# Performance work log

Measured on AMD Instinct MI355X. Metric: run time of the kernel, lower is better.

Reference implementation:

```python
import jax, jax.numpy as jnp
import numpy as np

SEQ, B, IN, H, L = 512, 64, 128, 256, 6
STDV = 1.0 / (H ** 0.5)


def setup_inputs() -> dict:
    key = jax.random.key(0)
    ks = jax.random.split(key, 7)
    return {
        "x": jax.random.normal(ks[0], (SEQ, B, IN), jnp.float32),
        "h0": jax.random.normal(ks[1], (L, B, H), jnp.float32),
        "w_ih0": jax.random.uniform(ks[2], (3 * H, IN), jnp.float32, -STDV, STDV),
        "w_ih_rest": jax.random.uniform(ks[3], (L - 1, 3 * H, H), jnp.float32, -STDV, STDV),
        "w_hh": jax.random.uniform(ks[4], (L, 3 * H, H), jnp.float32, -STDV, STDV),
        "b_ih": jax.random.uniform(ks[5], (L, 3 * H), jnp.float32, -STDV, STDV),
        "b_hh": jax.random.uniform(ks[6], (L, 3 * H), jnp.float32, -STDV, STDV),
    }


def _gru_layer(x, h0, w_ih, w_hh, b_ih, b_hh):
    # Precompute input-side gate projections for all timesteps: (S, B, 3H)
    xg = jnp.einsum("sbi,gi->sbg", x, w_ih) + b_ih

    def step(h, xg_t):
        hg = h @ w_hh.T + b_hh  # (B, 3H)
        xr, xz, xn = jnp.split(xg_t, 3, axis=-1)
        hr, hz, hn = jnp.split(hg, 3, axis=-1)
        r = jax.nn.sigmoid(xr + hr)
        z = jax.nn.sigmoid(xz + hz)
        n = jnp.tanh(xn + r * hn)
        h_new = (1.0 - z) * n + z * h
        return h_new, h_new

    h_n, ys = jax.lax.scan(step, h0, xg)
    return ys, h_n


def reference(x, h0, w_ih0, w_ih_rest, w_hh, b_ih, b_hh):
    cur = x
    h_finals = []
    for i in range(L):
        w_ih = w_ih0 if i == 0 else w_ih_rest[i - 1]
        cur, h_n = _gru_layer(cur, h0[i], w_ih, w_hh[i], b_ih[i], b_hh[i])
        h_finals.append(h_n)
    return cur, jnp.stack(h_finals, axis=0)
```

## Files before the change

### kernel.cpp

```cpp
#include <hip/hip_runtime.h>

#define SEQ 512
#define BB 64
#define IN_DIM 128
#define HH 256
#define NL 6
#define G3 768
#define CHUNK 8
#define NCH (SEQ/CHUNK)
#define FSTR 16

typedef short short8 __attribute__((ext_vector_type(8)));
typedef short short4v __attribute__((ext_vector_type(4)));
typedef float f32x4 __attribute__((ext_vector_type(4)));

#define FR_SH ((size_t)5*4*CHUNK*BB*HH)
#define XG_SH ((size_t)NL*2*CHUNK*G3*BB)
#define FLAGS_OFF_B ((FR_SH + XG_SH)*2)
#define NFLAG_INTS (16 + (24 + 96)*FSTR)

__device__ __forceinline__ short f2bf(float f) {
    unsigned u = __builtin_bit_cast(unsigned, f);
    u += 0x7fffu + ((u >> 16) & 1u);
    return (short)(u >> 16);
}
__device__ __forceinline__ float b2f(short s) {
    unsigned u = ((unsigned)(unsigned short)s) << 16;
    return __builtin_bit_cast(float, u);
}
__device__ __forceinline__ float sigm(float v) { return __fdividef(1.f, 1.f + __expf(-v)); }
__device__ __forceinline__ float tanh_f(float v) { float e = __expf(2.f * v); return 1.f - __fdividef(2.f, e + 1.f); }

__device__ __forceinline__ short8 pack_row(const float* p) {
    float4 a = *(const float4*)p;
    float4 c = *(const float4*)(p + 4);
    short8 v;
    v[0] = f2bf(a.x); v[1] = f2bf(a.y); v[2] = f2bf(a.z); v[3] = f2bf(a.w);
    v[4] = f2bf(c.x); v[5] = f2bf(c.y); v[6] = f2bf(c.z); v[7] = f2bf(c.w);
    return v;
}

__global__ __launch_bounds__(512, 1) void gru_persist(
    const float* __restrict__ x, const float* __restrict__ h0,
    const float* __restrict__ w_ih0, const float* __restrict__ w_ih_rest,
    const float* __restrict__ w_hh, const float* __restrict__ b_ih,
    const float* __restrict__ b_hh, float* __restrict__ y,
    short* __restrict__ fring, short* __restrict__ xg, int* __restrict__ flags)
{
    extern __shared__ char smem[];
    const int tid = threadIdx.x;
    const unsigned long long ddl = __builtin_amdgcn_s_memrealtime() + 800000000ull;

    const int xcc = __builtin_amdgcn_s_getreg(20 | (31 << 11)) & 0xf;
    if (xcc >= NL) return;
    __shared__ int s_slot;
    if (tid == 0) s_slot = __hip_atomic_fetch_add(&flags[xcc], 1, __ATOMIC_RELAXED, __HIP_MEMORY_SCOPE_AGENT);
    __syncthreads();
    const int slot = s_slot;
    if (slot >= 20) return;

    const int l = xcc;
    const int lane = tid & 63;
    const int wave = tid >> 6;
    const int q = lane >> 4;
    const int jj = lane & 15;

    int* recF  = flags + 16;
    int* projF = flags + 16 + 24 * FSTR;

    if (slot < 4) {
        const int g = slot;
        char* sWn = smem;
        char* sHB = smem + 131072;

        const float* whh = w_hh + (size_t)l * G3 * HH;
        short8 Wreg[4][8];
        #pragma unroll
        for (int i = 0; i < 4; ++i) {
            int row = (i >> 1) * HH + 32 * wave + 16 * (i & 1) + jj;
            #pragma unroll
            for (int kt = 0; kt < 8; ++kt)
                Wreg[i][kt] = pack_row(whh + (size_t)row * HH + kt * 32 + q * 8);
        }
        #pragma unroll
        for (int i2 = 0; i2 < 2; ++i2) {
            int row = 512 + 32 * wave + 16 * i2 + jj;
            #pragma unroll
            for (int kt = 0; kt < 8; ++kt) {
                short8 v = pack_row(whh + (size_t)row * HH + kt * 32 + q * 8);
                *(short8*)(sWn + ((size_t)(wave * 2 + i2) * 8 + kt) * 1024 + lane * 16) = v;
            }
        }
        float bhr[2], bhz[2], bhn2[2];
        #pragma unroll
        for (int jt2 = 0; jt2 < 2; ++jt2) {
            int j = 32 * wave + 16 * jt2 + jj;
            bhr[jt2]  = b_hh[l * G3 + j];
            bhz[jt2]  = b_hh[l * G3 + 256 + j];
            bhn2[jt2] = b_hh[l * G3 + 512 + j];
        }
        float hcur[2][4];
        #pragma unroll
        for (int jt2 = 0; jt2 < 2; ++jt2) {
            int j = 32 * wave + 16 * jt2 + jj;
            #pragma unroll
            for (int r = 0; r < 4; ++r)
                hcur[jt2][r] = h0[((size_t)l * BB + 16 * g + 4 * q + r) * HH + j];
        }
        for (int i = tid; i < 16 * 256; i += 512) {
            int b = i >> 8, j = i & 255;
            short hb = f2bf(h0[((size_t)l * BB + 16 * g + b) * HH + j]);
            *(short*)(sHB + b * 512 + ((2 * j) ^ ((b & 7) << 4))) = hb;
        }
        __syncthreads();

        for (int c = 0; c < NCH; ++c) {
            if (wave == 0) {
                const int* pa = nullptr; int tgt = 0;
                if (lane < 8) { pa = &projF[(l * 16 + 2 * lane + (g >> 1)) * FSTR]; tgt = c + 1; }
                else if (lane < 16 && l < NL - 1) { pa = &projF[((l + 1) * 16 + 2 * (lane - 8) + (g >> 1)) * FSTR]; tgt = c - 3; }
                int it = 0;
                for (;;) {
                    bool ok = true;
                    if (pa) ok = __hip_atomic_load((int*)pa, __ATOMIC_RELAXED, __HIP_MEMORY_SCOPE_AGENT) >= tgt;
                    if (__ballot(ok) == ~0ull) break;
                    __builtin_amdgcn_s_sleep(1);
                    if (((++it) & 63) == 0 && __builtin_amdgcn_s_memrealtime() > ddl) break;
                }
                __builtin_amdgcn_fence(__ATOMIC_ACQUIRE, "agent");
            }
            __syncthreads();

            const short* xgc = xg + ((size_t)(l * 2 + (c & 1)) * CHUNK) * G3 * BB;
            short* frc = (l < NL - 1) ? fring + ((size_t)(l * 4 + (c & 3)) * CHUNK) * BB * HH : nullptr;

            for (int ts = 0; ts < CHUNK; ++ts) {
                const int t = c * CHUNK + ts;
                const int cur = t & 1, nxt = cur ^ 1;
                f32x4 acc[6] = {};
                #pragma unroll
                for (int kt = 0; kt < 8; ++kt) {
                    short8 af = *(const short8*)(sHB + cur * 8192 + (lane & 15) * 512
                                 + ((kt * 64 + q * 16) ^ ((lane & 7) << 4)));
                    acc[0] = __builtin_amdgcn_mfma_f32_16x16x32_bf16(af, Wreg[0][kt], acc[0], 0, 0, 0);
                    acc[1] = __builtin_amdgcn_mfma_f32_16x16x32_bf16(af, Wreg[1][kt], acc[1], 0, 0, 0);
                    acc[2] = __builtin_amdgcn_mfma_f32_16x16x32_bf16(af, Wreg[2][kt], acc[2], 0, 0, 0);
                    acc[3] = __builtin_amdgcn_mfma_f32_16x16x32_bf16(af, Wreg[3][kt], acc[3], 0, 0, 0);
                    short8 w4 = *(const short8*)(sWn + ((size_t)(wave * 2 + 0) * 8 + kt) * 1024 + lane * 16);
                    short8 w5 = *(const short8*)(sWn + ((size_t)(wave * 2 + 1) * 8 + kt) * 1024 + lane * 16);
                    acc[4] = __builtin_amdgcn_mfma_f32_16x16x32_bf16(af, w4, acc[4], 0, 0, 0);
                    acc[5] = __builtin_amdgcn_mfma_f32_16x16x32_bf16(af, w5, acc[5], 0, 0, 0);
                }
                const short* xgt = xgc + (size_t)ts * G3 * BB;
                float* ydst = y + (size_t)t * BB * HH;
                #pragma unroll
                for (int jt2 = 0; jt2 < 2; ++jt2) {
                    int j = 32 * wave + 16 * jt2 + jj;
                    short4v xr = *(const short4v*)(xgt + (size_t)j * BB + 16 * g + 4 * q);
                    short4v xz = *(const short4v*)(xgt + (size_t)(256 + j) * BB + 16 * g + 4 * q);
                    short4v xn = *(const short4v*)(xgt + (size_t)(512 + j) * BB + 16 * g + 4 * q);
                    #pragma unroll
                    for (int r = 0; r < 4; ++r) {
                        int b = 4 * q + r;
                        float rg = sigm(acc[jt2][r] + b2f(xr[r]) + bhr[jt2]);
                        float zg = sigm(acc[2 + jt2][r] + b2f(xz[r]) + bhz[jt2]);
                        float ng = tanh_f(b2f(xn[r]) + rg * (acc[4 + jt2][r] + bhn2[jt2]));
                        float hn = ng + zg * (hcur[jt2][r] - ng);
                        hcur[jt2][r] = hn;
                        short hb = f2bf(hn);
                        *(short*)(sHB + nxt * 8192 + b * 512 + ((2 * j) ^ ((b & 7) << 4))) = hb;
                        if (l < NL - 1) frc[((size_t)ts * BB + 16 * g + b) * HH + j] = hb;
                        else            ydst[((size_t)16 * g + b) * HH + j] = hn;
                    }
                }
                __syncthreads();
            }
            if (tid == 0)
                __hip_atomic_store(&recF[(l * 4 + g) * FSTR], c + 1, __ATOMIC_RELEASE, __HIP_MEMORY_SCOPE_AGENT);
        }
        #pragma unroll
        for (int jt2 = 0; jt2 < 2; ++jt2) {
            int j = 32 * wave + 16 * jt2 + jj;
            #pragma unroll
            for (int r = 0; r < 4; ++r)
                y[(size_t)SEQ * BB * HH + (size_t)l * BB * HH + ((size_t)16 * g + 4 * q + r) * HH + j] = hcur[jt2][r];
        }
    } else {
        const int p = slot - 4;
        const int t_p = p >> 1;
        const int bh = p & 1;
        const int KIN = (l == 0) ? IN_DIM : HH;
        const int KTp = (l == 0) ? 4 : 8;
        char* sWp = smem;

        const float* wih = (l == 0) ? w_ih0 : (w_ih_rest + (size_t)(l - 1) * G3 * HH);
        short8 Wp[4][8];
        #pragma unroll
        for (int i = 0; i < 4; ++i) {
            int row = (6 * wave + i) * 16 + jj;
            for (int kt = 0; kt < KTp; ++kt)
                Wp[i][kt] = pack_row(wih + (size_t)row * KIN + kt * 32 + q * 8);
        }
        #pragma unroll
        for (int i2 = 0; i2 < 2; ++i2) {
            int row = (6 * wave + 4 + i2) * 16 + jj;
            for (int kt = 0; kt < KTp; ++kt) {
                short8 v = pack_row(wih + (size_t)row * KIN + kt * 32 + q * 8);
                *(short8*)(sWp + ((size_t)(wave * 2 + i2) * 8 + kt) * 1024 + lane * 16) = v;
            }
        }
        float bias[6];
        #pragma unroll
        for (int i = 0; i < 6; ++i)
            bias[i] = b_ih[l * G3 + (6 * wave + i) * 16 + jj];
        __syncthreads();

        for (int c = 0; c < NCH; ++c) {
            if (wave == 0) {
                const int* pa = nullptr; int tgt = 0;
                if (lane < 2) { if (l > 0) { pa = &recF[((l - 1) * 4 + 2 * bh + lane) * FSTR]; tgt = c + 1; } }
                else if (lane < 4) { pa = &recF[(l * 4 + 2 * bh + (lane - 2)) * FSTR]; tgt = c - 1; }
                int it = 0;
                for (;;) {
                    bool ok = true;
                    if (pa) ok = __hip_atomic_load((int*)pa, __ATOMIC_RELAXED, __HIP_MEMORY_SCOPE_AGENT) >= tgt;
                    if (__ballot(ok) == ~0ull) break;
                    __builtin_amdgcn_s_sleep(1);
                    if (((++it) & 63) == 0 && __builtin_amdgcn_s_memrealtime() > ddl) break;
                }
                __builtin_amdgcn_fence(__ATOMIC_ACQUIRE, "agent");
            }
            __syncthreads();

            short* xgd = xg + ((size_t)(l * 2 + (c & 1)) * CHUNK + t_p) * G3 * BB;
            const short* frs = (l > 0)
                ? fring + ((size_t)((l - 1) * 4 + (c & 3)) * CHUNK + t_p) * BB * HH : nullptr;

            #pragma unroll
            for (int mt2 = 0; mt2 < 2; ++mt2) {
                const int bgl = 32 * bh + 16 * mt2 + (lane & 15);
                f32x4 acc[6] = {};
                for (int kt = 0; kt < KTp; ++kt) {
                    short8 af;
                    if (l == 0) {
                        const float* ap = x + ((size_t)(c * CHUNK + t_p) * BB + bgl) * IN_DIM + kt * 32 + q * 8;
                        af = pack_row(ap);
                    } else {
                        af = *(const short8*)(frs + (size_t)bgl * HH + kt * 32 + q * 8);
                    }
                    acc[0] = __builtin_amdgcn_mfma_f32_16x16x32_bf16(af, Wp[0][kt], acc[0], 0, 0, 0);
                    acc[1] = __builtin_amdgcn_mfma_f32_16x16x32_bf16(af, Wp[1][kt], acc[1], 0, 0, 0);
                    acc[2] = __builtin_amdgcn_mfma_f32_16x16x32_bf16(af, Wp[2][kt], acc[2], 0, 0, 0);
                    acc[3] = __builtin_amdgcn_mfma_f32_16x16x32_bf16(af, Wp[3][kt], acc[3], 0, 0, 0);
                    short8 w4 = *(const short8*)(sWp + ((size_t)(wave * 2 + 0) * 8 + kt) * 1024 + lane * 16);
                    short8 w5 = *(const short8*)(sWp + ((size_t)(wave * 2 + 1) * 8 + kt) * 1024 + lane * 16);
                    acc[4] = __builtin_amdgcn_mfma_f32_16x16x32_bf16(af, w4, acc[4], 0, 0, 0);
                    acc[5] = __builtin_amdgcn_mfma_f32_16x16x32_bf16(af, w5, acc[5], 0, 0, 0);
                }
                #pragma unroll
                for (int i = 0; i < 6; ++i) {
                    int j = (6 * wave + i) * 16 + jj;
                    short4v o;
                    o[0] = f2bf(acc[i][0] + bias[i]);
                    o[1] = f2bf(acc[i][1] + bias[i]);
                    o[2] = f2bf(acc[i][2] + bias[i]);
                    o[3] = f2bf(acc[i][3] + bias[i]);
                    *(short4v*)(xgd + (size_t)j * BB + 32 * bh + 16 * mt2 + 4 * q) = o;
                }
            }
            __syncthreads();
            if (tid == 0)
                __hip_atomic_store(&projF[(l * 16 + p) * FSTR], c + 1, __ATOMIC_RELEASE, __HIP_MEMORY_SCOPE_AGENT);
        }
    }
}

extern "C" void kernel_launch(void* const* d_in, const int* in_sizes, int n_in,
                              void* d_out, int out_size, void* d_ws, size_t ws_size,
                              hipStream_t stream) {
    (void)in_sizes; (void)n_in; (void)out_size; (void)ws_size;
    const float* x         = (const float*)d_in[0];
    const float* h0        = (const float*)d_in[1];
    const float* w_ih0     = (const float*)d_in[2];
    const float* w_ih_rest = (const float*)d_in[3];
    const float* w_hh      = (const float*)d_in[4];
    const float* b_ih      = (const float*)d_in[5];
    const float* b_hh      = (const float*)d_in[6];
    float* y = (float*)d_out;

    short* fring = (short*)d_ws;
    short* xgb   = fring + FR_SH;
    int*   flags = (int*)((char*)d_ws + FLAGS_OFF_B);

    (void)hipMemsetAsync(flags, 0, NFLAG_INTS * sizeof(int), stream);
    gru_persist<<<256, 512, 147456, stream>>>(
        x, h0, w_ih0, w_ih_rest, w_hh, b_ih, b_hh, y, fring, xgb, flags);
}
```

Measured before the change: 4.673 ms.

## Re-layout xg per batch group, prefetch gates early, coalesce recurrent output stores

The xg gate buffer is re-laid out so each 16-row batch group's gates are contiguous. The recurrent blocks now issue the xg loads with inline asm before the MFMA loop and wait on them only afterwards, so the loads overlap the matmul. Scattered per-element hidden-state writes to the ring and output are replaced by a coalesced 16-byte pass that reads the bf16 h back from shared memory after the barrier. Projection blocks preload their A fragments and skip the acquire fence for layer 0. In exchange, the final-layer y output is now written from the bf16-rounded h rather than fp32, the recurrent acquire fence is removed, and the inline-asm loads use sc0, which may risk visibility ordering.

```diff
diff --git a/kernel.cpp b/kernel.cpp
--- a/kernel.cpp
+++ b/kernel.cpp
@@ -15,9 +15,10 @@
 typedef float f32x4 __attribute__((ext_vector_type(4)));
 
 #define FR_SH ((size_t)5*4*CHUNK*BB*HH)
-#define XG_SH ((size_t)NL*2*CHUNK*G3*BB)
+#define XG_SH ((size_t)NL*2*CHUNK*4*G3*16)
 #define FLAGS_OFF_B ((FR_SH + XG_SH)*2)
 #define NFLAG_INTS (16 + (24 + 96)*FSTR)
+#define XGI(L,CS,TS,GI) (((((size_t)(L)*2+(CS))*CHUNK+(TS))*4+(GI))*((size_t)G3*16))
 
 __device__ __forceinline__ short f2bf(float f) {
     unsigned u = __builtin_bit_cast(unsigned, f);
@@ -38,6 +39,21 @@
     v[0] = f2bf(a.x); v[1] = f2bf(a.y); v[2] = f2bf(a.z); v[3] = f2bf(a.w);
     v[4] = f2bf(c.x); v[5] = f2bf(c.y); v[6] = f2bf(c.z); v[7] = f2bf(c.w);
     return v;
+}
+
+struct XgRegs { short4v r0, r1, z0, z1, n0, n1; };
+__device__ __forceinline__ XgRegs ld_xg(const short* pR, const short* pZ, const short* pN) {
+    XgRegs o;
+    asm volatile(
+        "global_load_dwordx2 %0, %6, off sc0\n\t"
+        "global_load_dwordx2 %1, %6, off offset:512 sc0\n\t"
+        "global_load_dwordx2 %2, %7, off sc0\n\t"
+        "global_load_dwordx2 %3, %7, off offset:512 sc0\n\t"
+        "global_load_dwordx2 %4, %8, off sc0\n\t"
+        "global_load_dwordx2 %5, %8, off offset:512 sc0"
+        : "=&v"(o.r0), "=&v"(o.r1), "=&v"(o.z0), "=&v"(o.z1), "=&v"(o.n0), "=&v"(o.n1)
+        : "v"(pR), "v"(pZ), "v"(pN) : "memory");
+    return o;
 }
 
 __global__ __launch_bounds__(512, 1) void gru_persist(
@@ -113,6 +129,9 @@
             *(short*)(sHB + b * 512 + ((2 * j) ^ ((b & 7) << 4))) = hb;
         }
         __syncthreads();
+
+        const int cb = tid >> 5;
+        const int cj0 = (tid & 31) * 8;
 
         for (int c = 0; c < NCH; ++c) {
             if (wave == 0) {
@@ -127,16 +146,19 @@
                     __builtin_amdgcn_s_sleep(1);
                     if (((++it) & 63) == 0 && __builtin_amdgcn_s_memrealtime() > ddl) break;
                 }
-                __builtin_amdgcn_fence(__ATOMIC_ACQUIRE, "agent");
             }
             __syncthreads();
 
-            const short* xgc = xg + ((size_t)(l * 2 + (c & 1)) * CHUNK) * G3 * BB;
             short* frc = (l < NL - 1) ? fring + ((size_t)(l * 4 + (c & 3)) * CHUNK) * BB * HH : nullptr;
 
             for (int ts = 0; ts < CHUNK; ++ts) {
                 const int t = c * CHUNK + ts;
                 const int cur = t & 1, nxt = cur ^ 1;
+
+                const short* xgts = xg + XGI(l, c & 1, ts, g);
+                const short* pR = xgts + (32 * wave + jj) * 16 + 4 * q;
+                XgRegs xr = ld_xg(pR, pR + 256 * 16, pR + 512 * 16);
+
                 f32x4 acc[6] = {};
                 #pragma unroll
                 for (int kt = 0; kt < 8; ++kt) {
@@ -151,30 +173,40 @@
                     acc[4] = __builtin_amdgcn_mfma_f32_16x16x32_bf16(af, w4, acc[4], 0, 0, 0);
                     acc[5] = __builtin_amdgcn_mfma_f32_16x16x32_bf16(af, w5, acc[5], 0, 0, 0);
                 }
-                const short* xgt = xgc + (size_t)ts * G3 * BB;
-                float* ydst = y + (size_t)t * BB * HH;
+                asm volatile("s_waitcnt vmcnt(0)" ::: "memory");
+
                 #pragma unroll
                 for (int jt2 = 0; jt2 < 2; ++jt2) {
                     int j = 32 * wave + 16 * jt2 + jj;
-                    short4v xr = *(const short4v*)(xgt + (size_t)j * BB + 16 * g + 4 * q);
-                    short4v xz = *(const short4v*)(xgt + (size_t)(256 + j) * BB + 16 * g + 4 * q);
-                    short4v xn = *(const short4v*)(xgt + (size_t)(512 + j) * BB + 16 * g + 4 * q);
+                    short4v xrv = jt2 ? xr.r1 : xr.r0;
+                    short4v xzv = jt2 ? xr.z1 : xr.z0;
+                    short4v xnv = jt2 ? xr.n1 : xr.n0;
                     #pragma unroll
                     for (int r = 0; r < 4; ++r) {
                         int b = 4 * q + r;
-                        float rg = sigm(acc[jt2][r] + b2f(xr[r]) + bhr[jt2]);
-                        float zg = sigm(acc[2 + jt2][r] + b2f(xz[r]) + bhz[jt2]);
-                        float ng = tanh_f(b2f(xn[r]) + rg * (acc[4 + jt2][r] + bhn2[jt2]));
+                        float rg = sigm(acc[jt2][r] + b2f(xrv[r]) + bhr[jt2]);
+                        float zg = sigm(acc[2 + jt2][r] + b2f(xzv[r]) + bhz[jt2]);
+                        float ng = tanh_f(b2f(xnv[r]) + rg * (acc[4 + jt2][r] + bhn2[jt2]));
                         float hn = ng + zg * (hcur[jt2][r] - ng);
                         hcur[jt2][r] = hn;
-                        short hb = f2bf(hn);
-                        *(short*)(sHB + nxt * 8192 + b * 512 + ((2 * j) ^ ((b & 7) << 4))) = hb;
-                        if (l < NL - 1) frc[((size_t)ts * BB + 16 * g + b) * HH + j] = hb;
-                        else            ydst[((size_t)16 * g + b) * HH + j] = hn;
+                        *(short*)(sHB + nxt * 8192 + b * 512 + ((2 * j) ^ ((b & 7) << 4))) = f2bf(hn);
                     }
                 }
                 __syncthreads();
-            }
+
+                short8 hv = *(const short8*)(sHB + nxt * 8192 + cb * 512 + ((2 * cj0) ^ ((cb & 7) << 4)));
+                if (l < NL - 1) {
+                    *(short8*)(frc + ((size_t)ts * BB + 16 * g + cb) * HH + cj0) = hv;
+                } else {
+                    float4 f0, f1;
+                    f0.x = b2f(hv[0]); f0.y = b2f(hv[1]); f0.z = b2f(hv[2]); f0.w = b2f(hv[3]);
+                    f1.x = b2f(hv[4]); f1.y = b2f(hv[5]); f1.z = b2f(hv[6]); f1.w = b2f(hv[7]);
+                    float* yd = y + ((size_t)t * BB + 16 * g + cb) * HH + cj0;
+                    *(float4*)yd = f0;
+                    *(float4*)(yd + 4) = f1;
+                }
+            }
+            __syncthreads();
             if (tid == 0)
                 __hip_atomic_store(&recF[(l * 4 + g) * FSTR], c + 1, __ATOMIC_RELEASE, __HIP_MEMORY_SCOPE_AGENT);
         }
@@ -228,26 +260,26 @@
                     __builtin_amdgcn_s_sleep(1);
                     if (((++it) & 63) == 0 && __builtin_amdgcn_s_memrealtime() > ddl) break;
                 }
-                __builtin_amdgcn_fence(__ATOMIC_ACQUIRE, "agent");
+                if (l > 0) __builtin_amdgcn_fence(__ATOMIC_ACQUIRE, "agent");
             }
             __syncthreads();
 
-            short* xgd = xg + ((size_t)(l * 2 + (c & 1)) * CHUNK + t_p) * G3 * BB;
             const short* frs = (l > 0)
                 ? fring + ((size_t)((l - 1) * 4 + (c & 3)) * CHUNK + t_p) * BB * HH : nullptr;
 
             #pragma unroll
             for (int mt2 = 0; mt2 < 2; ++mt2) {
                 const int bgl = 32 * bh + 16 * mt2 + (lane & 15);
+                short8 afv[8];
+                for (int kt = 0; kt < KTp; ++kt) {
+                    if (l == 0)
+                        afv[kt] = pack_row(x + ((size_t)(c * CHUNK + t_p) * BB + bgl) * IN_DIM + kt * 32 + q * 8);
+                    else
+                        afv[kt] = *(const short8*)(frs + (size_t)bgl * HH + kt * 32 + q * 8);
+                }
                 f32x4 acc[6] = {};
                 for (int kt = 0; kt < KTp; ++kt) {
-                    short8 af;
-                    if (l == 0) {
-                        const float* ap = x + ((size_t)(c * CHUNK + t_p) * BB + bgl) * IN_DIM + kt * 32 + q * 8;
-                        af = pack_row(ap);
-                    } else {
-                        af = *(const short8*)(frs + (size_t)bgl * HH + kt * 32 + q * 8);
-                    }
+                    short8 af = afv[kt];
                     acc[0] = __builtin_amdgcn_mfma_f32_16x16x32_bf16(af, Wp[0][kt], acc[0], 0, 0, 0);
                     acc[1] = __builtin_amdgcn_mfma_f32_16x16x32_bf16(af, Wp[1][kt], acc[1], 0, 0, 0);
                     acc[2] = __builtin_amdgcn_mfma_f32_16x16x32_bf16(af, Wp[2][kt], acc[2], 0, 0, 0);
@@ -257,15 +289,16 @@
                     acc[4] = __builtin_amdgcn_mfma_f32_16x16x32_bf16(af, w4, acc[4], 0, 0, 0);
                     acc[5] = __builtin_amdgcn_mfma_f32_16x16x32_bf16(af, w5, acc[5], 0, 0, 0);
                 }
+                short* xgd = xg + XGI(l, c & 1, t_p, 2 * bh + mt2);
                 #pragma unroll
                 for (int i = 0; i < 6; ++i) {
-                    int j = (6 * wave + i) * 16 + jj;
+                    int r = (6 * wave + i) * 16 + jj;
                     short4v o;
                     o[0] = f2bf(acc[i][0] + bias[i]);
                     o[1] = f2bf(acc[i][1] + bias[i]);
                     o[2] = f2bf(acc[i][2] + bias[i]);
                     o[3] = f2bf(acc[i][3] + bias[i]);
-                    *(short4v*)(xgd + (size_t)j * BB + 32 * bh + 16 * mt2 + 4 * q) = o;
+                    *(short4v*)(xgd + (size_t)r * 16 + 4 * q) = o;
                 }
             }
             __syncthreads();
```

Result: faster. 4.095 ms (-12.4%).
